# Kernel optimization log

Measured on AMD Instinct MI355X. Metric: run time of the kernel, lower is better.

Reference implementation:

```python
import jax, jax.numpy as jnp
import numpy as np

SIZE = 11
SIGMA = 1.5
CHANNELS = 1
C1 = 0.01 ** 2
C2 = 0.03 ** 2


def _gaussian_kernel(size, sigma, channels):
    # 1D gaussian, outer product, normalized; depthwise kernel [C,1,k,k]
    coords = np.arange(size, dtype=np.float32) - (size - 1) / 2.0
    g = np.exp(-(coords ** 2) / (2.0 * sigma ** 2))
    g = g / g.sum()
    k2d = np.outer(g, g).astype(np.float32)
    k = np.tile(k2d[None, None], (channels, 1, 1, 1))  # [C,1,k,k]
    return jnp.asarray(k)


def _depthwise_conv(x, kernel):
    # x: [B,C,H,W], kernel: [C,1,k,k] -> SAME-padded depthwise conv
    pad = SIZE // 2
    return jax.lax.conv_general_dilated(
        x, kernel,
        window_strides=(1, 1),
        padding=[(pad, pad), (pad, pad)],
        dimension_numbers=('NCHW', 'OIHW', 'NCHW'),
        feature_group_count=CHANNELS,
    )


def setup_inputs() -> dict:
    key = jax.random.key(0)
    k1, k2 = jax.random.split(key)
    img_1 = jax.random.uniform(k1, (16, 1, 1024, 1024), dtype=jnp.float32)
    img_2 = jax.random.uniform(k2, (16, 1, 1024, 1024), dtype=jnp.float32)
    kernel = _gaussian_kernel(SIZE, SIGMA, CHANNELS)
    return {"img_1": img_1, "img_2": img_2, "kernel": kernel}


def reference(img_1, img_2, kernel):
    mu_x = _depthwise_conv(img_1, kernel)
    mu_y = _depthwise_conv(img_2, kernel)
    mu_x2 = mu_x * mu_x
    mu_y2 = mu_y * mu_y
    sigma_x2 = _depthwise_conv(img_1 * img_1, kernel) - mu_x2
    sigma_y2 = _depthwise_conv(img_2 * img_2, kernel) - mu_y2
    sigma_xy = _depthwise_conv(img_1 * img_2, kernel) - mu_x * mu_y
    ssim = ((2 * mu_x * mu_y + C1) * (2 * sigma_xy + C2)) / (
        (mu_x2 + mu_y2 + C1) * (sigma_x2 + sigma_y2 + C2))
    return jnp.mean(ssim)
```

## Files before the change

kernel.cpp:

```cpp
#include <hip/hip_runtime.h>

#define H 1024
#define W 1024
#define K 11
#define RAD 5
#define ROWS 64
#define NIN (ROWS + K - 1)
#define BW 256

typedef float v2f __attribute__((ext_vector_type(2)));

__global__ void zero_out_kernel(float* out) {
    if (threadIdx.x == 0) out[0] = 0.0f;
}

__device__ __forceinline__ float4 ld4u(const float* p) {
    float4 v;
    __builtin_memcpy(&v, p, sizeof(float4));
    return v;
}

__device__ __forceinline__ v2f pkfma(v2f a, v2f b, v2f c) {
    return __builtin_elementwise_fma(a, b, c);
}

template<bool FAST>
__device__ __forceinline__ void load_row(const float* __restrict__ r1,
                                         const float* __restrict__ r2,
                                         int col, float* x, float* y) {
    if (FAST) {
        const float* a1 = r1 + (col - RAD);
        const float* a2 = r2 + (col - RAD);
        float4 v0 = ld4u(a1), v1 = ld4u(a1 + 4), v2 = ld4u(a1 + 8);
        float4 u0 = ld4u(a2), u1 = ld4u(a2 + 4), u2 = ld4u(a2 + 8);
        x[0]=v0.x; x[1]=v0.y; x[2]=v0.z; x[3]=v0.w;
        x[4]=v1.x; x[5]=v1.y; x[6]=v1.z; x[7]=v1.w;
        x[8]=v2.x; x[9]=v2.y; x[10]=v2.z; x[11]=v2.w;
        y[0]=u0.x; y[1]=u0.y; y[2]=u0.z; y[3]=u0.w;
        y[4]=u1.x; y[5]=u1.y; y[6]=u1.z; y[7]=u1.w;
        y[8]=u2.x; y[9]=u2.y; y[10]=u2.z; y[11]=u2.w;
    } else {
        #pragma unroll
        for (int m = 0; m < 12; ++m) {
            const int gc = col - RAD + m;
            const bool ok = (unsigned)gc < (unsigned)W;
            x[m] = ok ? r1[gc] : 0.0f;
            y[m] = ok ? r2[gc] : 0.0f;
        }
    }
}

template<bool FAST>
__device__ __forceinline__ float run_strip(const float* __restrict__ p1,
                                           const float* __restrict__ p2,
                                           int col, int rin0, const float* gw) {
    v2f  rmu[K], rsq[K];
    float rxy[K];
    float acc = 0.0f;
    const float C1 = 1e-4f;
    const float C2 = 9e-4f;

    for (int base = 0; base < NIN; base += K) {
        #pragma unroll
        for (int p = 0; p < K; ++p) {
            const int i = base + p;
            if (i < NIN) {
                const int r  = rin0 + i;
                const int rr = min(max(r, 0), H - 1);
                const float s = ((unsigned)r < (unsigned)H) ? 1.0f : 0.0f;

                float x[12], y[12];
                load_row<FAST>(p1 + (size_t)rr * W, p2 + (size_t)rr * W, col, x, y);

                v2f amx = {0.f,0.f}, amy = {0.f,0.f};
                v2f axx = {0.f,0.f}, ayy = {0.f,0.f}, axy = {0.f,0.f};
                #pragma unroll
                for (int e = 0; e < 5; ++e) {
                    v2f w2 = { gw[2*e], gw[2*e+1] };
                    v2f xp = { x[2*e], x[2*e+1] };
                    v2f yp = { y[2*e], y[2*e+1] };
                    v2f wxp = w2 * xp;
                    v2f wyp = w2 * yp;
                    amx += wxp;
                    amy += wyp;
                    axx = pkfma(wxp, xp, axx);
                    ayy = pkfma(wyp, yp, ayy);
                    axy = pkfma(wxp, yp, axy);
                }
                const float twx = gw[10] * x[10];
                const float twy = gw[10] * y[10];
                const float hmx = (amx.x + amx.y) + twx;
                const float hmy = (amy.x + amy.y) + twy;
                const float hxx = fmaf(twx, x[10], axx.x + axx.y);
                const float hyy = fmaf(twy, y[10], ayy.x + ayy.y);
                const float hxy = fmaf(twx, y[10], axy.x + axy.y);

                v2f s2 = { s, s };
                rmu[p] = s2 * (v2f){ hmx, hmy };
                rsq[p] = s2 * (v2f){ hxx, hyy };
                rxy[p] = s * hxy;

                if (i >= K - 1) {
                    v2f mu = {0.f,0.f}, sq = {0.f,0.f};
                    float xy = 0.f;
                    #pragma unroll
                    for (int j = 0; j < K; ++j) {
                        const int sl = (p + 1 + j) % K;
                        const float w = gw[j];
                        v2f w2 = { w, w };
                        mu = pkfma(w2, rmu[sl], mu);
                        sq = pkfma(w2, rsq[sl], sq);
                        xy = fmaf(w, rxy[sl], xy);
                    }
                    v2f m2 = mu * mu;
                    const float mxy  = mu.x * mu.y;
                    v2f sg = sq - m2;
                    const float sxyv = xy - mxy;
                    const float num = fmaf(2.0f, mxy,  C1) * fmaf(2.0f, sxyv, C2);
                    const float den = (m2.x + m2.y + C1) * (sg.x + sg.y + C2);
                    acc += num * __builtin_amdgcn_rcpf(den);
                }
            }
        }
    }
    return acc;
}

__launch_bounds__(256, 2)
__global__ void ssim_kernel(const float* __restrict__ img1,
                            const float* __restrict__ img2,
                            const float* __restrict__ kern,
                            float* __restrict__ out,
                            float inv_n) {
    __shared__ float wsum[4];

    const int tid = threadIdx.x;
    const int col = blockIdx.x * BW + tid;
    const int ry0 = blockIdx.y * ROWS;
    const int b   = blockIdx.z;

    float gw[K];
    #pragma unroll
    for (int t = 0; t < K; ++t) {
        float s = 0.0f;
        #pragma unroll
        for (int j = 0; j < K; ++j) s += kern[t * K + j];
        gw[t] = __int_as_float(__builtin_amdgcn_readfirstlane(__float_as_int(s)));
    }

    const float* __restrict__ p1 = img1 + (size_t)b * H * W;
    const float* __restrict__ p2 = img2 + (size_t)b * H * W;
    const int rin0 = ry0 - RAD;

    const bool colfast = (col >= RAD) && (col + RAD + 1 < W);
    const unsigned long long bal = __ballot(colfast);
    float acc;
    if (bal == ~0ULL) {
        acc = run_strip<true>(p1, p2, col, rin0, gw);
    } else {
        acc = run_strip<false>(p1, p2, col, rin0, gw);
    }

    for (int off = 32; off > 0; off >>= 1)
        acc += __shfl_down(acc, off, 64);
    if ((tid & 63) == 0) wsum[tid >> 6] = acc;
    __syncthreads();
    if (tid == 0) {
        const float s = wsum[0] + wsum[1] + wsum[2] + wsum[3];
        atomicAdd(out, s * inv_n);
    }
}

extern "C" void kernel_launch(void* const* d_in, const int* in_sizes, int n_in,
                              void* d_out, int out_size, void* d_ws, size_t ws_size,
                              hipStream_t stream) {
    const float* img1 = (const float*)d_in[0];
    const float* img2 = (const float*)d_in[1];
    const float* kern = (const float*)d_in[2];
    float* out = (float*)d_out;

    const int B = in_sizes[0] / (H * W);
    const float inv_n = 1.0f / ((float)B * (float)H * (float)W);

    zero_out_kernel<<<dim3(1), dim3(64), 0, stream>>>(out);

    dim3 grid(W / BW, H / ROWS, B);
    ssim_kernel<<<grid, dim3(256), 0, stream>>>(img1, img2, kern, out, inv_n);
}
```

Before: 233.0 us.

## Merge x²+y² sums, prefetch next row, add row-interior fast path, halve strip

Horizontal pass now accumulates x² and y² into one combined sum, since only sigma_x2+sigma_y2 is used. That packs the vertical pass into two v2f registers instead of five values. Each row is software-prefetched one iteration ahead to hide load latency, and blocks whose rows are all in bounds skip the border masking multiply. The strip height drops from 64 to 32 rows, which doubles block count but raises the redundant halo rows from 10/64 to 10/32 of the loads. The prefetch also issues one extra clamped row load at the end.

Measured after the change: 266.2 us. 14.3% more time.

```diff
diff --git a/kernel.cpp b/kernel.cpp
--- a/kernel.cpp
+++ b/kernel.cpp
@@ -4,7 +4,7 @@
 #define W 1024
 #define K 11
 #define RAD 5
-#define ROWS 64
+#define ROWS 32
 #define NIN (ROWS + K - 1)
 #define BW 256
 
@@ -24,11 +24,11 @@
     return __builtin_elementwise_fma(a, b, c);
 }
 
-template<bool FAST>
+template<bool CFAST>
 __device__ __forceinline__ void load_row(const float* __restrict__ r1,
                                          const float* __restrict__ r2,
                                          int col, float* x, float* y) {
-    if (FAST) {
+    if (CFAST) {
         const float* a1 = r1 + (col - RAD);
         const float* a2 = r2 + (col - RAD);
         float4 v0 = ld4u(a1), v1 = ld4u(a1 + 4), v2 = ld4u(a1 + 8);
@@ -50,30 +50,36 @@
     }
 }
 
-template<bool FAST>
+template<bool CFAST, bool RFAST>
 __device__ __forceinline__ float run_strip(const float* __restrict__ p1,
                                            const float* __restrict__ p2,
                                            int col, int rin0, const float* gw) {
-    v2f  rmu[K], rsq[K];
-    float rxy[K];
+    v2f rmu[K], rsv[K];
     float acc = 0.0f;
-    const float C1 = 1e-4f;
-    const float C2 = 9e-4f;
+
+    float nx[12], ny[12];
+    {
+        const int rr = min(max(rin0, 0), H - 1);
+        load_row<CFAST>(p1 + (size_t)rr * W, p2 + (size_t)rr * W, col, nx, ny);
+    }
 
     for (int base = 0; base < NIN; base += K) {
         #pragma unroll
         for (int p = 0; p < K; ++p) {
             const int i = base + p;
             if (i < NIN) {
-                const int r  = rin0 + i;
-                const int rr = min(max(r, 0), H - 1);
-                const float s = ((unsigned)r < (unsigned)H) ? 1.0f : 0.0f;
-
                 float x[12], y[12];
-                load_row<FAST>(p1 + (size_t)rr * W, p2 + (size_t)rr * W, col, x, y);
+                #pragma unroll
+                for (int m = 0; m < 12; ++m) { x[m] = nx[m]; y[m] = ny[m]; }
+
+                {
+                    const int rr = min(max(rin0 + i + 1, 0), H - 1);
+                    load_row<CFAST>(p1 + (size_t)rr * W, p2 + (size_t)rr * W,
+                                    col, nx, ny);
+                }
 
                 v2f amx = {0.f,0.f}, amy = {0.f,0.f};
-                v2f axx = {0.f,0.f}, ayy = {0.f,0.f}, axy = {0.f,0.f};
+                v2f aq  = {0.f,0.f}, axy = {0.f,0.f};
                 #pragma unroll
                 for (int e = 0; e < 5; ++e) {
                     v2f w2 = { gw[2*e], gw[2*e+1] };
@@ -83,41 +89,44 @@
                     v2f wyp = w2 * yp;
                     amx += wxp;
                     amy += wyp;
-                    axx = pkfma(wxp, xp, axx);
-                    ayy = pkfma(wyp, yp, ayy);
+                    aq  = pkfma(wxp, xp, aq);
+                    aq  = pkfma(wyp, yp, aq);
                     axy = pkfma(wxp, yp, axy);
                 }
                 const float twx = gw[10] * x[10];
                 const float twy = gw[10] * y[10];
                 const float hmx = (amx.x + amx.y) + twx;
                 const float hmy = (amy.x + amy.y) + twy;
-                const float hxx = fmaf(twx, x[10], axx.x + axx.y);
-                const float hyy = fmaf(twy, y[10], ayy.x + ayy.y);
+                const float hq  = fmaf(twx, x[10], fmaf(twy, y[10], aq.x + aq.y));
                 const float hxy = fmaf(twx, y[10], axy.x + axy.y);
 
-                v2f s2 = { s, s };
-                rmu[p] = s2 * (v2f){ hmx, hmy };
-                rsq[p] = s2 * (v2f){ hxx, hyy };
-                rxy[p] = s * hxy;
+                if (RFAST) {
+                    rmu[p] = (v2f){ hmx, hmy };
+                    rsv[p] = (v2f){ hq,  hxy };
+                } else {
+                    const int r = rin0 + i;
+                    const float s = ((unsigned)r < (unsigned)H) ? 1.0f : 0.0f;
+                    v2f s2 = { s, s };
+                    rmu[p] = s2 * (v2f){ hmx, hmy };
+                    rsv[p] = s2 * (v2f){ hq,  hxy };
+                }
 
                 if (i >= K - 1) {
-                    v2f mu = {0.f,0.f}, sq = {0.f,0.f};
-                    float xy = 0.f;
+                    v2f mu = {0.f,0.f}, sv = {0.f,0.f};
                     #pragma unroll
                     for (int j = 0; j < K; ++j) {
                         const int sl = (p + 1 + j) % K;
-                        const float w = gw[j];
-                        v2f w2 = { w, w };
+                        v2f w2 = { gw[j], gw[j] };
                         mu = pkfma(w2, rmu[sl], mu);
-                        sq = pkfma(w2, rsq[sl], sq);
-                        xy = fmaf(w, rxy[sl], xy);
+                        sv = pkfma(w2, rsv[sl], sv);
                     }
                     v2f m2 = mu * mu;
                     const float mxy  = mu.x * mu.y;
-                    v2f sg = sq - m2;
-                    const float sxyv = xy - mxy;
-                    const float num = fmaf(2.0f, mxy,  C1) * fmaf(2.0f, sxyv, C2);
-                    const float den = (m2.x + m2.y + C1) * (sg.x + sg.y + C2);
+                    const float musq = m2.x + m2.y;
+                    const float sg   = sv.x - musq;
+                    const float sxyv = sv.y - mxy;
+                    const float num = fmaf(2.0f, mxy,  1e-4f) * fmaf(2.0f, sxyv, 9e-4f);
+                    const float den = (musq + 1e-4f) * (sg + 9e-4f);
                     acc += num * __builtin_amdgcn_rcpf(den);
                 }
             }
@@ -152,13 +161,17 @@
     const float* __restrict__ p2 = img2 + (size_t)b * H * W;
     const int rin0 = ry0 - RAD;
 
+    const bool rfast = (rin0 >= 0) && (rin0 + NIN <= H);
     const bool colfast = (col >= RAD) && (col + RAD + 1 < W);
     const unsigned long long bal = __ballot(colfast);
+
     float acc;
     if (bal == ~0ULL) {
-        acc = run_strip<true>(p1, p2, col, rin0, gw);
+        acc = rfast ? run_strip<true,  true >(p1, p2, col, rin0, gw)
+                    : run_strip<true,  false>(p1, p2, col, rin0, gw);
     } else {
-        acc = run_strip<false>(p1, p2, col, rin0, gw);
+        acc = rfast ? run_strip<false, true >(p1, p2, col, rin0, gw)
+                    : run_strip<false, false>(p1, p2, col, rin0, gw);
     }
 
     for (int off = 32; off > 0; off >>= 1)
```
